# Kernel optimization log

Measured on AMD Instinct MI355X. Metric: run time of the kernel, lower is better.

## Reference

```python
import math
import jax, jax.numpy as jnp
import numpy as np

MUL = 8      # multiplicity of 0e and 1o in irreps_in/out
KS = 5       # kernel spatial extent (diameter 5, steps 1 -> coords -2..2)
NB = 5       # num_radial_basis
RAD = 2.5    # diameter / 2


def _sus(t):
    # e3nn sus(x) = exp(-1/x) for x>0 else 0
    return jnp.where(t > 0.0, jnp.exp(-1.0 / jnp.where(t > 0.0, t, 1.0)), 0.0)


def _emb_sh():
    c = jnp.arange(-2.0, 3.0)
    lat = jnp.stack(jnp.meshgrid(c, c, c, indexing='ij'), axis=-1)  # (5,5,5,3)
    d = jnp.linalg.norm(lat, axis=-1)
    # soft_one_hot_linspace(basis='smooth_finite', cutoff=True)
    values = jnp.linspace(0.0, RAD, NB + 2)
    step = values[1] - values[0]
    diff = (d[..., None] - values[1:-1]) / step
    emb = 1.14136 * math.exp(2.0) * _sus(diff + 1.0) * _sus(1.0 - diff)  # (5,5,5,NB)
    # real spherical harmonics, lmax=2, normalize=True, normalization='component'
    safe = jnp.where(d > 0.0, d, 1.0)[..., None]
    u = jnp.where(d[..., None] > 0.0, lat / safe, 0.0)
    x, y, z = u[..., 0], u[..., 1], u[..., 2]
    s3, s5, s15 = math.sqrt(3.0), math.sqrt(5.0), math.sqrt(15.0)
    sh = jnp.stack([
        jnp.ones_like(x),
        s3 * x, s3 * y, s3 * z,
        s15 * x * z, s15 * x * y,
        s5 * (y * y - 0.5 * (x * x + z * z)),
        s15 * y * z, (s15 / 2.0) * (z * z - x * x),
    ], axis=-1)  # (5,5,5,9)
    return emb, sh


def _c121():
    # Clebsch-Gordan (w3j) for 1o x 2e -> 1o in the real e3nn basis, built from the
    # orthonormal symmetric-traceless matrix basis matching the l=2 SH component order.
    s2, s6 = math.sqrt(2.0), math.sqrt(6.0)
    S = np.zeros((5, 3, 3))
    S[0, 0, 2] = S[0, 2, 0] = 1.0 / s2            # xz
    S[1, 0, 1] = S[1, 1, 0] = 1.0 / s2            # xy
    S[2] = np.diag([-1.0, 2.0, -1.0]) / s6        # 2y^2 - x^2 - z^2
    S[3, 1, 2] = S[3, 2, 1] = 1.0 / s2            # yz
    S[4] = np.diag([-1.0, 0.0, 1.0]) / s2         # z^2 - x^2
    # w3j(1,2,1)[m,j,k] = S[j,m,k]/sqrt(5)  (fully symmetric since l1+l2+l3 even)
    return jnp.asarray(np.transpose(S, (1, 0, 2)) / math.sqrt(5.0), dtype=jnp.float32)


def _build_kernel(weight, emb, sh, c121, dtype):
    g = (KS, KS, KS)
    W = (emb @ weight) / float(KS * KS * KS)  # (5,5,5,320)
    w1, w2, w3, w4, w5 = [W[..., 64 * i:64 * (i + 1)].reshape(g + (MUL, MUL)) for i in range(5)]
    sh0, sh1, sh2 = sh[..., 0], sh[..., 1:4], sh[..., 4:9]
    pw0 = math.sqrt(1.0 / 16.0)   # output 0e: alpha=1, fan_in=8+8
    pw1 = math.sqrt(3.0 / 24.0)   # output 1o: alpha=3, fan_in=8+8+8
    inv_s3 = 1.0 / math.sqrt(3.0)
    K00 = pw0 * sh0[..., None, None] * w1                                   # (g,u,w)
    K01 = (pw1 * inv_s3) * jnp.einsum('xyzuw,xyzk->xyzuwk', w2, sh1)        # (g,u,w,k)
    K10 = (pw0 * inv_s3) * jnp.einsum('xyzuw,xyzm->xyzumw', w4, sh1)        # (g,u,m,w)
    T = jnp.einsum('xyzj,mjk->xyzmk', sh2, c121)                            # (g,m,k)
    eye3 = jnp.eye(3, dtype=dtype)
    K11 = pw1 * (inv_s3 * jnp.einsum('xyzuw,mk->xyzumwk', sh0[..., None, None] * w3, eye3)
                 + jnp.einsum('xyzuw,xyzmk->xyzumwk', w5, T))               # (g,u,m,w,k)
    D = 4 * MUL
    kern = jnp.zeros(g + (D, D), dtype=dtype)
    kern = kern.at[..., :MUL, :MUL].set(K00)
    kern = kern.at[..., :MUL, MUL:].set(K01.reshape(g + (MUL, 3 * MUL)))
    kern = kern.at[..., MUL:, :MUL].set(K10.reshape(g + (3 * MUL, MUL)))
    kern = kern.at[..., MUL:, MUL:].set(K11.reshape(g + (3 * MUL, 3 * MUL)))
    return jnp.transpose(kern, (4, 3, 0, 1, 2))  # 'xyzio->oixyz'


def reference(x, weight, w_sc0, w_sc1):
    emb, sh = _emb_sh()
    c121 = _c121()
    kern = _build_kernel(weight, emb, sh, c121, x.dtype)
    B, _, X, Y, Z = x.shape
    inv_s8 = 1.0 / math.sqrt(MUL)
    # self-connection: e3nn Linear, 0e->0e and 1o->1o blocks
    x0 = x[:, :MUL]
    x1 = x[:, MUL:].reshape(B, MUL, 3, X, Y, Z)
    sc0 = inv_s8 * jnp.einsum('uv,buxyz->bvxyz', w_sc0, x0)
    sc1 = inv_s8 * jnp.einsum('uv,bumxyz->bvmxyz', w_sc1, x1).reshape(B, 3 * MUL, X, Y, Z)
    sc = jnp.concatenate([sc0, sc1], axis=1)
    conv = jax.lax.conv_general_dilated(
        x, kern, window_strides=(1, 1, 1), padding=[(2, 2)] * 3,
        dimension_numbers=('NCDHW', 'OIDHW', 'NCDHW'))
    return sc + conv


def setup_inputs() -> dict:
    key = jax.random.key(0)
    k1, k2, k3, k4 = jax.random.split(key, 4)
    return {
        'x': jax.random.normal(k1, (2, 32, 64, 64, 64), dtype=jnp.float32),
        'weight': jax.random.normal(k2, (NB, 5 * MUL * MUL), dtype=jnp.float32),
        'w_sc0': jax.random.normal(k3, (MUL, MUL), dtype=jnp.float32),
        'w_sc1': jax.random.normal(k4, (MUL, MUL), dtype=jnp.float32),
    }
```

## Files before the change

### kernel.cpp

```cpp
#include <hip/hip_runtime.h>
#include <math.h>

typedef __attribute__((ext_vector_type(8))) short short8;
typedef __attribute__((ext_vector_type(4))) float f32x4;
typedef __attribute__((ext_vector_type(16))) float f32x16;

#define NTAP 125
#define DCH 32

static __device__ __forceinline__ unsigned short f2bf(float f) {
    union { float f; unsigned u; } v; v.f = f;
    unsigned u = v.u;
    return (unsigned short)((u + 0x7FFFu + ((u >> 16) & 1u)) >> 16);
}

static __device__ __forceinline__ void gld_lds16(const void* g, void* l) {
    __builtin_amdgcn_global_load_lds(
        (const __attribute__((address_space(1))) unsigned int*)g,
        (__attribute__((address_space(3))) unsigned int*)l, 16, 0, 0);
}

__global__ __launch_bounds__(128) void build_pack(
    const float* __restrict__ weight,
    const float* __restrict__ w_sc0,
    const float* __restrict__ w_sc1,
    unsigned short* __restrict__ kwb)
{
    const int t = blockIdx.x;
    const int dx = t / 25, dy = (t / 5) % 5, dz = t % 5;
    const float px = dx - 2.0f, py = dy - 2.0f, pz = dz - 2.0f;
    const float d = sqrtf(px * px + py * py + pz * pz);

    const float stepv = 2.5f / 6.0f;
    const float embc = 1.14136f * expf(2.0f);
    float emb[5];
#pragma unroll
    for (int n = 0; n < 5; ++n) {
        float diff = (d - stepv * (float)(n + 1)) / stepv;
        float a = diff + 1.0f, bb = 1.0f - diff;
        float v = 0.0f;
        if (a > 0.0f && bb > 0.0f)
            v = embc * expf(-1.0f / a) * expf(-1.0f / bb);
        emb[n] = v;
    }

    const float inv_d = (d > 0.0f) ? 1.0f / d : 0.0f;
    const float ux = px * inv_d, uy = py * inv_d, uz = pz * inv_d;
    const float s3 = 1.73205081f, s5 = 2.23606798f, s15 = 3.87298335f;
    float sh[9];
    sh[0] = 1.0f;
    sh[1] = s3 * ux; sh[2] = s3 * uy; sh[3] = s3 * uz;
    sh[4] = s15 * ux * uz;
    sh[5] = s15 * ux * uy;
    sh[6] = s5 * (uy * uy - 0.5f * (ux * ux + uz * uz));
    sh[7] = s15 * uy * uz;
    sh[8] = 0.5f * s15 * (uz * uz - ux * ux);

    const float i_s2 = 0.70710678f, i_s6 = 0.40824829f, i_s5 = 0.44721360f;
    float T[3][3];
    T[0][0] = i_s5 * (-sh[6] * i_s6 - sh[8] * i_s2);
    T[0][1] = i_s5 * (sh[5] * i_s2);
    T[0][2] = i_s5 * (sh[4] * i_s2);
    T[1][0] = T[0][1];
    T[1][1] = i_s5 * (2.0f * sh[6] * i_s6);
    T[1][2] = i_s5 * (sh[7] * i_s2);
    T[2][0] = T[0][2];
    T[2][1] = T[1][2];
    T[2][2] = i_s5 * (-sh[6] * i_s6 + sh[8] * i_s2);

    __shared__ float Wt[320];
    __shared__ float kws[1024];
    for (int col = threadIdx.x; col < 320; col += 128) {
        float a = 0.0f;
#pragma unroll
        for (int n = 0; n < 5; ++n) a += emb[n] * weight[n * 320 + col];
        Wt[col] = a * (1.0f / 125.0f);
    }
    __syncthreads();

    const float pw0 = 0.25f;
    const float pw1 = 0.35355339f;
    const float inv_s3 = 0.57735027f;
    const float inv_s8 = 0.35355339f;

    for (int idx = threadIdx.x; idx < 1024; idx += 128) {
        const int o = idx >> 5, i = idx & 31;
        float val;
        if (o < 8) {
            if (i < 8) {
                val = pw0 * Wt[i * 8 + o];
            } else {
                const int u = (i - 8) / 3, m = (i - 8) % 3;
                val = pw0 * inv_s3 * Wt[192 + u * 8 + o] * sh[1 + m];
            }
        } else {
            const int v = (o - 8) / 3, k = (o - 8) % 3;
            if (i < 8) {
                val = pw1 * inv_s3 * Wt[64 + i * 8 + v] * sh[1 + k];
            } else {
                const int u = (i - 8) / 3, m = (i - 8) % 3;
                float tv = Wt[256 + u * 8 + v] * T[m][k];
                if (m == k) tv += inv_s3 * Wt[128 + u * 8 + v];
                val = pw1 * tv;
            }
        }
        if (t == 62) {
            if (o < 8 && i < 8) {
                val += inv_s8 * w_sc0[i * 8 + o];
            } else if (o >= 8 && i >= 8) {
                const int u = (i - 8) / 3, m = (i - 8) % 3;
                const int v = (o - 8) / 3, k = (o - 8) % 3;
                if (m == k) val += inv_s8 * w_sc1[u * 8 + v];
            }
        }
        kws[i * 32 + o] = val;
    }
    __syncthreads();

    const int tid = threadIdx.x;
    const int kh = tid >> 6, l = tid & 63;
    const int co = l & 31;
    const int cib = kh * 16 + (l >> 5) * 8;
    unsigned short v[8];
#pragma unroll
    for (int j = 0; j < 8; ++j)
        v[j] = f2bf(kws[(cib + j) * 32 + co]);
    uint4 o;
    o.x = (unsigned)v[0] | ((unsigned)v[1] << 16);
    o.y = (unsigned)v[2] | ((unsigned)v[3] << 16);
    o.z = (unsigned)v[4] | ((unsigned)v[5] << 16);
    o.w = (unsigned)v[6] | ((unsigned)v[7] << 16);
    *reinterpret_cast<uint4*>(kwb + ((size_t)(t * 2 + kh) * 64 + l) * 8) = o;
}

__global__ __launch_bounds__(256) void xpose(
    const float* __restrict__ x, unsigned short* __restrict__ xt)
{
    const int xx = blockIdx.x, yy = blockIdx.y, b = blockIdx.z;
    const int t = threadIdx.x;
    const int z = t & 63, part = t >> 6;
    const float* src = x + ((((size_t)b * 32) * 64 + xx) * 64 + yy) * 64 + z;
    unsigned short v[8];
#pragma unroll
    for (int j = 0; j < 8; ++j)
        v[j] = f2bf(src[(size_t)(part * 8 + j) * 262144]);
    uint4 o;
    o.x = (unsigned)v[0] | ((unsigned)v[1] << 16);
    o.y = (unsigned)v[2] | ((unsigned)v[3] << 16);
    o.z = (unsigned)v[4] | ((unsigned)v[5] << 16);
    o.w = (unsigned)v[6] | ((unsigned)v[7] << 16);
    *reinterpret_cast<uint4*>(
        xt + ((((size_t)b * 64 + xx) * 64 + yy) * 64 + z) * 32 + part * 8) = o;
}

__global__ void zero_fill(float4* p) {
    p[threadIdx.x] = make_float4(0.f, 0.f, 0.f, 0.f);
}

__global__ __launch_bounds__(512, 2) void conv_mfma(
    const unsigned short* __restrict__ xt,
    const unsigned short* __restrict__ kwb,
    const unsigned short* __restrict__ zpage,
    float* __restrict__ out)
{
    extern __shared__ unsigned short smem[];
    char* lds = (char*)smem;
    const unsigned lds0 = (unsigned)__builtin_amdgcn_groupstaticsize();

    const int tid = threadIdx.x;
    const int lane = tid & 63;
    const int wv = tid >> 6;
    const int oyp = wv >> 1, zh = wv & 1;
    const int x0 = blockIdx.x * 4, y0 = blockIdx.y * 8;
    const int b = blockIdx.z;
    const int l31 = lane & 31, hi = lane >> 5;

    int abase[5][2];
#pragma unroll
    for (int dz = 0; dz < 5; ++dz) {
        const int s = zh * 32 + l31 + dz;
#pragma unroll
        for (int kh = 0; kh < 2; ++kh) {
            const int cph = (kh * 2 + hi) ^ ((s >> 1) & 3);
            abase[dz][kh] = (int)lds0 +
                51200 + ((((oyp * 2 * 68 + s) << 2) | cph) << 4);
        }
    }
    const unsigned baddr = lds0 + (unsigned)(lane * 16);

    int srow[5]; int soff[5]; bool szok[5];
#pragma unroll
    for (int p = 0; p < 5; ++p) {
        const int c = tid + p * 512;
        const int row = c / 272;
        const int rem = c - row * 272;
        const int slot = rem >> 2;
        const int clog = (rem & 3) ^ ((slot >> 1) & 3);
        const int z = slot - 2;
        srow[p] = row;
        szok[p] = ((unsigned)z < 64u);
        soff[p] = row * 2048 + z * 32 + clog * 8;
    }

    int bsrc[7];
#pragma unroll
    for (int k = 0; k < 7; ++k) {
        const int c = tid + k * 512;
        const int tp = c >> 7, rem = c & 127;
        const int dxx = tp / 5, dzz = tp - dxx * 5;
        bsrc[k] = (dxx * 25 + dzz) * 128 + rem;
    }

    auto issue_bs = [&](int dy) {
#pragma unroll
        for (int k = 0; k < 7; ++k) {
            const int c0 = wv * 64 + k * 512;
            if (c0 < 3200) {
                gld_lds16(kwb + ((size_t)(bsrc[k] + dy * 640)) * 8,
                          lds + c0 * 16);
            }
        }
    };

    auto issue_slab = [&](int dyn, int xln, int dstoff) {
        const int yyb = y0 + dyn - 2;
        const int xx = x0 + xln - 2;
        const bool xok = ((unsigned)xx < 64u);
        const long long xyb =
            (long long)(b * 64 + xx) * 131072 + (long long)yyb * 2048;
        char* dst = lds + 51200 + dstoff;
#pragma unroll
        for (int p = 0; p < 4; ++p) {
            const int yy = yyb + srow[p];
            const bool ok = xok && ((unsigned)yy < 64u) && szok[p];
            const unsigned short* src = ok ? (xt + xyb + soff[p]) : zpage;
            gld_lds16(src, dst + (wv * 64 + p * 512) * 16);
        }
        if (wv < 2) {
            const int yy = yyb + srow[4];
            const bool ok = xok && ((unsigned)yy < 64u) && szok[4];
            const unsigned short* src = ok ? (xt + xyb + soff[4]) : zpage;
            gld_lds16(src, dst + (wv * 64 + 2048) * 16);
        }
    };

    auto wait_keep_slab = [&]() {
        if (wv < 2) asm volatile("s_waitcnt vmcnt(5)" ::: "memory");
        else        asm volatile("s_waitcnt vmcnt(4)" ::: "memory");
    };

    f32x16 acc[2][4];
#pragma unroll
    for (int oyi = 0; oyi < 2; ++oyi)
#pragma unroll
        for (int ox = 0; ox < 4; ++ox)
#pragma unroll
            for (int e = 0; e < 16; ++e) acc[oyi][ox][e] = 0.0f;

    issue_bs(0);
    __builtin_amdgcn_sched_barrier(0);
    issue_slab(0, 0, 0);
    __builtin_amdgcn_sched_barrier(0);
    issue_slab(0, 1, 34816);
    __builtin_amdgcn_sched_barrier(0);
    wait_keep_slab();
    __builtin_amdgcn_s_barrier();

    int rd = 0;
    int prev = 69632;

    for (int dy = 0; dy < 5; ++dy) {
#pragma unroll
        for (int xl = 0; xl < 8; ++xl) {
            const bool bdry = (xl == 0) && (dy > 0);
            if (bdry) {
                issue_bs(dy);
                __builtin_amdgcn_sched_barrier(0);
            }
            if (!(dy == 4 && xl >= 6)) {
                const int ndy = (xl >= 6) ? dy + 1 : dy;
                const int nxl = (xl >= 6) ? xl - 6 : xl + 2;
                issue_slab(ndy, nxl, prev);
                __builtin_amdgcn_sched_barrier(0);
            }
            if (bdry) {
                wait_keep_slab();
                __builtin_amdgcn_s_barrier();
            }

            const int oxlo = (xl - 4 > 0) ? (xl - 4) : 0;
            const int oxhi = (xl < 3) ? xl : 3;
            const int S = 2 + (oxhi - oxlo + 1);

            short8 A0[2], A1[2], B[2][4];

            {
                const unsigned aa = (unsigned)(abase[0][0] + rd);
                asm volatile("ds_read_b128 %0, %1"
                             : "=&v"(A0[0]) : "v"(aa));
                asm volatile("ds_read_b128 %0, %1 offset:4352"
                             : "=&v"(A1[0]) : "v"(aa));
#pragma unroll
                for (int ox = 0; ox < 4; ++ox) {
                    if (ox < oxlo || ox > oxhi) continue;
                    const unsigned bb = baddr +
                        (unsigned)((((xl - ox) * 5 + 0) * 2 + 0) << 10);
                    asm volatile("ds_read_b128 %0, %1"
                                 : "=&v"(B[0][ox]) : "v"(bb));
                }
            }
#pragma unroll
            for (int g = 0; g < 10; ++g) {
                const int cs = g & 1;
                if (g < 9) {
                    const int g1 = g + 1;
                    const int dz1 = g1 >> 1, kh1 = g1 & 1, ns = g1 & 1;
                    const unsigned aa = (unsigned)(abase[dz1][kh1] + rd);
                    asm volatile("ds_read_b128 %0, %1"
                                 : "=&v"(A0[ns]) : "v"(aa));
                    asm volatile("ds_read_b128 %0, %1 offset:4352"
                                 : "=&v"(A1[ns]) : "v"(aa));
#pragma unroll
                    for (int ox = 0; ox < 4; ++ox) {
                        if (ox < oxlo || ox > oxhi) continue;
                        const unsigned bb = baddr +
                            (unsigned)((((xl - ox) * 5 + dz1) * 2 + kh1)
                                       << 10);
                        asm volatile("ds_read_b128 %0, %1"
                                     : "=&v"(B[ns][ox]) : "v"(bb));
                    }
                    if (S == 3)
                        asm volatile("s_waitcnt lgkmcnt(3)" ::: "memory");
                    else if (S == 4)
                        asm volatile("s_waitcnt lgkmcnt(4)" ::: "memory");
                    else if (S == 5)
                        asm volatile("s_waitcnt lgkmcnt(5)" ::: "memory");
                    else
                        asm volatile("s_waitcnt lgkmcnt(6)" ::: "memory");
                } else {
                    asm volatile("s_waitcnt lgkmcnt(0)" ::: "memory");
                }
                __builtin_amdgcn_sched_barrier(0);
#pragma unroll
                for (int ox = 0; ox < 4; ++ox) {
                    if (ox < oxlo || ox > oxhi) continue;
                    acc[0][ox] = __builtin_amdgcn_mfma_f32_32x32x16_bf16(
                        A0[cs], B[cs][ox], acc[0][ox], 0, 0, 0);
                    acc[1][ox] = __builtin_amdgcn_mfma_f32_32x32x16_bf16(
                        A1[cs], B[cs][ox], acc[1][ox], 0, 0, 0);
                }
            }

            if (dy == 4 && xl >= 6) {
                asm volatile("s_waitcnt vmcnt(0)" ::: "memory");
            } else {
                wait_keep_slab();
            }
            if (!(dy == 4 && xl == 7))
                __builtin_amdgcn_s_barrier();

            const int tmp = rd;
            rd = (rd == 69632) ? 0 : rd + 34816;
            prev = tmp;
        }
    }

#pragma unroll
    for (int oyi = 0; oyi < 2; ++oyi) {
        const int yy = y0 + oyp * 2 + oyi;
#pragma unroll
        for (int ox = 0; ox < 4; ++ox) {
            float* base = out +
                ((((size_t)b * 32 + l31) * 64 + (x0 + ox)) * 64 + yy) * 64 +
                zh * 32 + hi * 4;
#pragma unroll
            for (int rq = 0; rq < 4; ++rq) {
                f32x4 v = { acc[oyi][ox][rq * 4 + 0], acc[oyi][ox][rq * 4 + 1],
                            acc[oyi][ox][rq * 4 + 2], acc[oyi][ox][rq * 4 + 3] };
                *reinterpret_cast<f32x4*>(base + rq * 8) = v;
            }
        }
    }
}

extern "C" void kernel_launch(void* const* d_in, const int* in_sizes, int n_in,
                              void* d_out, int out_size, void* d_ws, size_t ws_size,
                              hipStream_t stream) {
    const float* x      = (const float*)d_in[0];
    const float* weight = (const float*)d_in[1];
    const float* w_sc0  = (const float*)d_in[2];
    const float* w_sc1  = (const float*)d_in[3];
    float* out = (float*)d_out;

    char* ws = (char*)d_ws;
    unsigned short* xt  = (unsigned short*)ws;
    unsigned short* kwb = (unsigned short*)(ws + 33554432);
    unsigned short* zpg = (unsigned short*)(ws + 33810432);

    (void)hipFuncSetAttribute((const void*)conv_mfma,
                              hipFuncAttributeMaxDynamicSharedMemorySize,
                              155648);

    hipLaunchKernelGGL(build_pack, dim3(NTAP), dim3(128), 0, stream,
                       weight, w_sc0, w_sc1, kwb);
    hipLaunchKernelGGL(xpose, dim3(64, 64, 2), dim3(256), 0, stream, x, xt);
    hipLaunchKernelGGL(zero_fill, dim3(1), dim3(256), 0, stream, (float4*)zpg);
    hipLaunchKernelGGL(conv_mfma, dim3(16, 8, 2), dim3(512), 155648, stream,
                       xt, kwb, zpg, out);
}
```

Before: 150.6 us.

## Halve block to 4 waves, each computing 4 output rows for more B-fragment reuse

```diff
diff --git a/kernel.cpp b/kernel.cpp
--- a/kernel.cpp
+++ b/kernel.cpp
@@ -157,7 +157,7 @@
     p[threadIdx.x] = make_float4(0.f, 0.f, 0.f, 0.f);
 }
 
-__global__ __launch_bounds__(512, 2) void conv_mfma(
+__global__ __launch_bounds__(256, 1) void conv_mfma(
     const unsigned short* __restrict__ xt,
     const unsigned short* __restrict__ kwb,
     const unsigned short* __restrict__ zpage,
@@ -170,7 +170,7 @@
     const int tid = threadIdx.x;
     const int lane = tid & 63;
     const int wv = tid >> 6;
-    const int oyp = wv >> 1, zh = wv & 1;
+    const int oyq = wv >> 1, zh = wv & 1;
     const int x0 = blockIdx.x * 4, y0 = blockIdx.y * 8;
     const int b = blockIdx.z;
     const int l31 = lane & 31, hi = lane >> 5;
@@ -183,15 +183,15 @@
         for (int kh = 0; kh < 2; ++kh) {
             const int cph = (kh * 2 + hi) ^ ((s >> 1) & 3);
             abase[dz][kh] = (int)lds0 +
-                51200 + ((((oyp * 2 * 68 + s) << 2) | cph) << 4);
+                51200 + ((((oyq * 4 * 68 + s) << 2) | cph) << 4);
         }
     }
     const unsigned baddr = lds0 + (unsigned)(lane * 16);
 
-    int srow[5]; int soff[5]; bool szok[5];
-#pragma unroll
-    for (int p = 0; p < 5; ++p) {
-        const int c = tid + p * 512;
+    int srow[9]; int soff[9]; bool szok[9];
+#pragma unroll
+    for (int p = 0; p < 9; ++p) {
+        const int c = tid + p * 256;
         const int row = c / 272;
         const int rem = c - row * 272;
         const int slot = rem >> 2;
@@ -202,10 +202,10 @@
         soff[p] = row * 2048 + z * 32 + clog * 8;
     }
 
-    int bsrc[7];
-#pragma unroll
-    for (int k = 0; k < 7; ++k) {
-        const int c = tid + k * 512;
+    int bsrc[13];
+#pragma unroll
+    for (int k = 0; k < 13; ++k) {
+        const int c = tid + k * 256;
         const int tp = c >> 7, rem = c & 127;
         const int dxx = tp / 5, dzz = tp - dxx * 5;
         bsrc[k] = (dxx * 25 + dzz) * 128 + rem;
@@ -213,12 +213,13 @@
 
     auto issue_bs = [&](int dy) {
 #pragma unroll
-        for (int k = 0; k < 7; ++k) {
-            const int c0 = wv * 64 + k * 512;
-            if (c0 < 3200) {
-                gld_lds16(kwb + ((size_t)(bsrc[k] + dy * 640)) * 8,
-                          lds + c0 * 16);
-            }
+        for (int k = 0; k < 12; ++k) {
+            gld_lds16(kwb + ((size_t)(bsrc[k] + dy * 640)) * 8,
+                      lds + (wv * 64 + k * 256) * 16);
+        }
+        if (wv < 2) {
+            gld_lds16(kwb + ((size_t)(bsrc[12] + dy * 640)) * 8,
+                      lds + (wv * 64 + 3072) * 16);
         }
     };
 
@@ -230,28 +231,28 @@
             (long long)(b * 64 + xx) * 131072 + (long long)yyb * 2048;
         char* dst = lds + 51200 + dstoff;
 #pragma unroll
-        for (int p = 0; p < 4; ++p) {
+        for (int p = 0; p < 8; ++p) {
             const int yy = yyb + srow[p];
             const bool ok = xok && ((unsigned)yy < 64u) && szok[p];
             const unsigned short* src = ok ? (xt + xyb + soff[p]) : zpage;
-            gld_lds16(src, dst + (wv * 64 + p * 512) * 16);
+            gld_lds16(src, dst + (wv * 64 + p * 256) * 16);
         }
         if (wv < 2) {
-            const int yy = yyb + srow[4];
-            const bool ok = xok && ((unsigned)yy < 64u) && szok[4];
-            const unsigned short* src = ok ? (xt + xyb + soff[4]) : zpage;
+            const int yy = yyb + srow[8];
+            const bool ok = xok && ((unsigned)yy < 64u) && szok[8];
+            const unsigned short* src = ok ? (xt + xyb + soff[8]) : zpage;
             gld_lds16(src, dst + (wv * 64 + 2048) * 16);
         }
     };
 
     auto wait_keep_slab = [&]() {
-        if (wv < 2) asm volatile("s_waitcnt vmcnt(5)" ::: "memory");
-        else        asm volatile("s_waitcnt vmcnt(4)" ::: "memory");
+        if (wv < 2) asm volatile("s_waitcnt vmcnt(9)" ::: "memory");
+        else        asm volatile("s_waitcnt vmcnt(8)" ::: "memory");
     };
 
-    f32x16 acc[2][4];
-#pragma unroll
-    for (int oyi = 0; oyi < 2; ++oyi)
+    f32x16 acc[4][4];
+#pragma unroll
+    for (int oyi = 0; oyi < 4; ++oyi)
 #pragma unroll
         for (int ox = 0; ox < 4; ++ox)
 #pragma unroll
@@ -290,16 +291,20 @@
 
             const int oxlo = (xl - 4 > 0) ? (xl - 4) : 0;
             const int oxhi = (xl < 3) ? xl : 3;
-            const int S = 2 + (oxhi - oxlo + 1);
-
-            short8 A0[2], A1[2], B[2][4];
+            const int S = 4 + (oxhi - oxlo + 1);
+
+            short8 A[2][4], B[2][4];
 
             {
                 const unsigned aa = (unsigned)(abase[0][0] + rd);
                 asm volatile("ds_read_b128 %0, %1"
-                             : "=&v"(A0[0]) : "v"(aa));
+                             : "=&v"(A[0][0]) : "v"(aa));
                 asm volatile("ds_read_b128 %0, %1 offset:4352"
-                             : "=&v"(A1[0]) : "v"(aa));
+                             : "=&v"(A[0][1]) : "v"(aa));
+                asm volatile("ds_read_b128 %0, %1 offset:8704"
+                             : "=&v"(A[0][2]) : "v"(aa));
+                asm volatile("ds_read_b128 %0, %1 offset:13056"
+                             : "=&v"(A[0][3]) : "v"(aa));
 #pragma unroll
                 for (int ox = 0; ox < 4; ++ox) {
                     if (ox < oxlo || ox > oxhi) continue;
@@ -317,9 +322,13 @@
                     const int dz1 = g1 >> 1, kh1 = g1 & 1, ns = g1 & 1;
                     const unsigned aa = (unsigned)(abase[dz1][kh1] + rd);
                     asm volatile("ds_read_b128 %0, %1"
-                                 : "=&v"(A0[ns]) : "v"(aa));
+                                 : "=&v"(A[ns][0]) : "v"(aa));
                     asm volatile("ds_read_b128 %0, %1 offset:4352"
-                                 : "=&v"(A1[ns]) : "v"(aa));
+                                 : "=&v"(A[ns][1]) : "v"(aa));
+                    asm volatile("ds_read_b128 %0, %1 offset:8704"
+                                 : "=&v"(A[ns][2]) : "v"(aa));
+                    asm volatile("ds_read_b128 %0, %1 offset:13056"
+                                 : "=&v"(A[ns][3]) : "v"(aa));
 #pragma unroll
                     for (int ox = 0; ox < 4; ++ox) {
                         if (ox < oxlo || ox > oxhi) continue;
@@ -329,14 +338,14 @@
                         asm volatile("ds_read_b128 %0, %1"
                                      : "=&v"(B[ns][ox]) : "v"(bb));
                     }
-                    if (S == 3)
-                        asm volatile("s_waitcnt lgkmcnt(3)" ::: "memory");
-                    else if (S == 4)
-                        asm volatile("s_waitcnt lgkmcnt(4)" ::: "memory");
-                    else if (S == 5)
+                    if (S == 5)
                         asm volatile("s_waitcnt lgkmcnt(5)" ::: "memory");
+                    else if (S == 6)
+                        asm volatile("s_waitcnt lgkmcnt(6)" ::: "memory");
+                    else if (S == 7)
+                        asm volatile("s_waitcnt lgkmcnt(7)" ::: "memory");
                     else
-                        asm volatile("s_waitcnt lgkmcnt(6)" ::: "memory");
+                        asm volatile("s_waitcnt lgkmcnt(8)" ::: "memory");
                 } else {
                     asm volatile("s_waitcnt lgkmcnt(0)" ::: "memory");
                 }
@@ -344,10 +353,11 @@
 #pragma unroll
                 for (int ox = 0; ox < 4; ++ox) {
                     if (ox < oxlo || ox > oxhi) continue;
-                    acc[0][ox] = __builtin_amdgcn_mfma_f32_32x32x16_bf16(
-                        A0[cs], B[cs][ox], acc[0][ox], 0, 0, 0);
-                    acc[1][ox] = __builtin_amdgcn_mfma_f32_32x32x16_bf16(
-                        A1[cs], B[cs][ox], acc[1][ox], 0, 0, 0);
+#pragma unroll
+                    for (int oyi = 0; oyi < 4; ++oyi) {
+                        acc[oyi][ox] = __builtin_amdgcn_mfma_f32_32x32x16_bf16(
+                            A[cs][oyi], B[cs][ox], acc[oyi][ox], 0, 0, 0);
+                    }
                 }
             }
 
@@ -366,8 +376,8 @@
     }
 
 #pragma unroll
-    for (int oyi = 0; oyi < 2; ++oyi) {
-        const int yy = y0 + oyp * 2 + oyi;
+    for (int oyi = 0; oyi < 4; ++oyi) {
+        const int yy = y0 + oyq * 4 + oyi;
 #pragma unroll
         for (int ox = 0; ox < 4; ++ox) {
             float* base = out +
@@ -405,6 +415,6 @@
                        weight, w_sc0, w_sc1, kwb);
     hipLaunchKernelGGL(xpose, dim3(64, 64, 2), dim3(256), 0, stream, x, xt);
     hipLaunchKernelGGL(zero_fill, dim3(1), dim3(256), 0, stream, (float4*)zpg);
-    hipLaunchKernelGGL(conv_mfma, dim3(16, 8, 2), dim3(512), 155648, stream,
+    hipLaunchKernelGGL(conv_mfma, dim3(16, 8, 2), dim3(256), 155648, stream,
                        xt, kwb, zpg, out);
 }
```

New measurement: 147.1 us. 1.02x faster.
